# Kernel optimization log

Hardware: AMD Instinct MI355X
Metric: run time of the kernel (lower is better)

Reference implementation:

```python
import jax, jax.numpy as jnp
import numpy as np

D_MODEL = 512
HIDDEN = 2 * D_MODEL
B, L = 8, 2048
R_MIN, R_MAX = 0.8, 0.99
LN_EPS = 1e-5


def setup_inputs() -> dict:
    key = jax.random.key(0)
    ks = jax.random.split(key, 12)
    x = jax.random.normal(ks[0], (B, L, D_MODEL), jnp.float32)
    mask = jnp.ones((B, L), jnp.float32)
    # LRU eigenvalue init, exactly as the torch __init__
    u1 = jax.random.uniform(ks[1], (HIDDEN,), jnp.float32)
    u2 = jax.random.uniform(ks[2], (HIDDEN,), jnp.float32)
    nu_log = jnp.log(-0.5 * jnp.log(u1 * (R_MAX ** 2 - R_MIN ** 2) + R_MIN ** 2))
    theta_log = jnp.log(u2 * 2.0 * np.pi)
    diag_lambda = jnp.exp(jax.lax.complex(-jnp.exp(nu_log), jnp.exp(theta_log)))
    gamma_log = jnp.log(jnp.sqrt(1.0 - jnp.abs(diag_lambda) ** 2))
    params_log = jnp.stack([nu_log, theta_log, gamma_log])  # (3, HIDDEN)
    s_in = 1.0 / np.sqrt(D_MODEL)
    s_out = 1.0 / np.sqrt(HIDDEN)
    # complex Linear weights (real+imag parts; trained weights are fully complex)
    W_in_re = jax.random.uniform(ks[3], (HIDDEN, D_MODEL), jnp.float32, -s_in, s_in)
    W_in_im = jax.random.uniform(ks[4], (HIDDEN, D_MODEL), jnp.float32, -s_in, s_in)
    b_in_re = jax.random.uniform(ks[5], (HIDDEN,), jnp.float32, -s_in, s_in)
    b_in_im = jax.random.uniform(ks[6], (HIDDEN,), jnp.float32, -s_in, s_in)
    W_out_re = jax.random.uniform(ks[7], (D_MODEL, HIDDEN), jnp.float32, -s_out, s_out)
    W_out_im = jax.random.uniform(ks[8], (D_MODEL, HIDDEN), jnp.float32, -s_out, s_out)
    b_out_re = jax.random.uniform(ks[9], (D_MODEL,), jnp.float32, -s_out, s_out)
    b_out_im = jax.random.uniform(ks[10], (D_MODEL,), jnp.float32, -s_out, s_out)
    ln_w = jnp.ones((D_MODEL,), jnp.float32)
    ln_b = jnp.zeros((D_MODEL,), jnp.float32)
    return dict(x=x, mask=mask, params_log=params_log,
                W_in_re=W_in_re, W_in_im=W_in_im, b_in_re=b_in_re, b_in_im=b_in_im,
                W_out_re=W_out_re, W_out_im=W_out_im, b_out_re=b_out_re, b_out_im=b_out_im,
                ln_w=ln_w, ln_b=ln_b)


def _lru_parallel_scan(h, lamb, mask, Bn, Ln, Dn):
    # log-depth doubling trick over complex diagonal recurrence (faithful port)
    log2_L = int(np.ceil(np.log2(Ln)))
    for i in range(1, log2_L + 1):
        l = 2 ** i
        h = h.reshape(Bn * Ln // l, l, Dn)
        m = mask.reshape(Bn * Ln // l, l)
        h1, h2 = h[:, : l // 2], h[:, l // 2 :]
        if i > 1:
            lamb = jnp.concatenate([lamb, lamb * lamb[-1]], axis=0)  # powers lam^1..lam^(l/2)
        h2 = h2 + lamb * h1[:, -1:] * m[:, l // 2 - 1 : l // 2, None]
        h = jnp.concatenate([h1, h2], axis=1)
    return h.reshape(Bn, Ln, Dn)


def reference(x, mask, params_log, W_in_re, W_in_im, b_in_re, b_in_im,
              W_out_re, W_out_im, b_out_re, b_out_im, ln_w, ln_b):
    nu, theta, gamma = jnp.exp(params_log)  # each (HIDDEN,)
    lamb = jnp.exp(jax.lax.complex(-nu, theta))[None, :]  # (1, HIDDEN)
    W_in = jax.lax.complex(W_in_re, W_in_im)
    b_in = jax.lax.complex(b_in_re, b_in_im)
    W_out = jax.lax.complex(W_out_re, W_out_im)
    b_out = jax.lax.complex(b_out_re, b_out_im)
    xc = x.astype(jnp.complex64)
    h = (jnp.einsum('bld,hd->blh', xc, W_in) + b_in) * gamma  # (B, L, HIDDEN) complex64
    Bn, Ln, Dn = h.shape
    h = _lru_parallel_scan(h, lamb, mask, Bn, Ln, Dn)
    y = (jnp.einsum('blh,dh->bld', h, W_out) + b_out).real + x  # dropout = identity (eval)
    mean = jnp.mean(y, axis=-1, keepdims=True)
    var = jnp.var(y, axis=-1, keepdims=True)
    return (y - mean) / jnp.sqrt(var + LN_EPS) * ln_w + ln_b
```

## Files before the change

### kernel.cpp

```cpp
#include <hip/hip_runtime.h>
#include <hip/hip_bf16.h>
#include <cstdint>
#include <cstddef>


typedef unsigned short u16;
typedef __attribute__((ext_vector_type(8))) short bf16x8;
typedef __attribute__((ext_vector_type(4))) float f32x4;

#define B_    8
#define L_    2048
#define D_    512
#define H_    1024
#define M_    (B_ * L_)
#define SEG_  64
#define T_    (L_ / SEG_)

__device__ __forceinline__ float b2f(u16 u) {
  union { unsigned int i; float f; } v; v.i = ((unsigned int)u) << 16; return v.f;
}
__device__ __forceinline__ u16 f2b(float f) {
  union { float f; unsigned int i; } v; v.f = f;
  unsigned int x = v.i;
  return (u16)((x + 0x7fffu + ((x >> 16) & 1u)) >> 16);
}

__device__ __forceinline__ void gl2lds16(const void* g, void* l) {
  __builtin_amdgcn_global_load_lds(
      (const __attribute__((address_space(1))) void*)g,
      (__attribute__((address_space(3))) void*)l, 16, 0, 0);
}

__device__ __forceinline__ int ksw8(int row, int c) {
  return (c ^ (row & 7)) & 7;
}

__global__ __launch_bounds__(256) void conv_f32_bf16(
    const float* __restrict__ in, u16* __restrict__ out, int n4)
{
  int i = blockIdx.x * 256 + threadIdx.x;
  if (i < n4) {
    float4 v = ((const float4*)in)[i];
    ushort4 o;
    o.x = f2b(v.x); o.y = f2b(v.y); o.z = f2b(v.z); o.w = f2b(v.w);
    ((ushort4*)out)[i] = o;
  }
}

__global__ __launch_bounds__(256) void prep_weights(
    const float* __restrict__ wire, const float* __restrict__ wiim,
    const float* __restrict__ wore, const float* __restrict__ woim,
    const float* __restrict__ bire, const float* __restrict__ biim,
    const float* __restrict__ params,
    u16* __restrict__ winb, u16* __restrict__ wcat, float* __restrict__ bb)
{
  int i = blockIdx.x * 256 + threadIdx.x;
  float g = expf(params[2 * H_ + (i >> 9)]);
  winb[i]           = f2b(wire[i] * g);
  winb[H_ * D_ + i] = f2b(wiim[i] * g);
  int d = i >> 10, c = i & 1023;
  wcat[(size_t)d * 2048 + c]        = f2b(wore[i]);
  wcat[(size_t)d * 2048 + 1024 + c] = f2b(-woim[i]);
  if (i < 2048) {
    float gb = expf(params[2 * H_ + (i & (H_ - 1))]);
    bb[i] = ((i < 1024) ? bire[i] : biim[i - 1024]) * gb;
  }
}

template <int MODE>
__global__ __launch_bounds__(256, 3) void gemm_bt(
    const u16* __restrict__ A, const u16* __restrict__ Bp, int K,
    void* __restrict__ outp, int ldc, const float* __restrict__ p0)
{
  __shared__ __align__(16) u16 sA[128 * 64];
  __shared__ __align__(16) u16 sB[128 * 64];

  const int tid  = threadIdx.x;
  const int lane = tid & 63;
  const int wave = tid >> 6;
  const int wm = wave >> 1, wn = wave & 1;
  const int m0 = blockIdx.x * 128;
  const int n0 = blockIdx.y * 128;

  f32x4 acc[4][4];
#pragma unroll
  for (int i = 0; i < 4; ++i)
#pragma unroll
    for (int j = 0; j < 4; ++j) { f32x4 z = {0.f, 0.f, 0.f, 0.f}; acc[i][j] = z; }

  const int q = lane >> 4;
  const int r = lane & 15;

  for (int k0 = 0; k0 < K; k0 += 64) {
#pragma unroll
    for (int it = 0; it < 4; ++it) {
      int ci  = it * 256 + tid;
      int row = ci >> 3;
      int kc  = ksw8(row, ci & 7);
      gl2lds16(A  + (size_t)(m0 + row) * K + k0 + kc * 8, &sA[ci * 8]);
      gl2lds16(Bp + (size_t)(n0 + row) * K + k0 + kc * 8, &sB[ci * 8]);
    }
    __syncthreads();

#pragma unroll
    for (int kk = 0; kk < 2; ++kk) {
      const int cs = kk * 4 + q;
      bf16x8 af[4], bfv[4];
#pragma unroll
      for (int mt = 0; mt < 4; ++mt) {
        int arow = wm * 64 + mt * 16 + r;
        int slot = arow * 8 + ksw8(arow, cs);
        af[mt] = *(const bf16x8*)&sA[slot * 8];
      }
#pragma unroll
      for (int nt = 0; nt < 4; ++nt) {
        int brow = wn * 64 + nt * 16 + r;
        int slot = brow * 8 + ksw8(brow, cs);
        bfv[nt] = *(const bf16x8*)&sB[slot * 8];
      }
#pragma unroll
      for (int mt = 0; mt < 4; ++mt)
#pragma unroll
        for (int nt = 0; nt < 4; ++nt)
          acc[mt][nt] = __builtin_amdgcn_mfma_f32_16x16x32_bf16(
              bfv[nt], af[mt], acc[mt][nt], 0, 0, 0);
    }
    __syncthreads();
  }

#pragma unroll
  for (int nt = 0; nt < 4; ++nt) {
    const int nb4 = n0 + wn * 64 + nt * 16 + q * 4;
    const float4 b4 = *(const float4*)&p0[nb4];
#pragma unroll
    for (int mt = 0; mt < 4; ++mt) {
      const int mg = m0 + wm * 64 + mt * 16 + r;
      if (MODE == 0) {
        ushort4 o;
        o.x = f2b(acc[mt][nt][0] + b4.x);
        o.y = f2b(acc[mt][nt][1] + b4.y);
        o.z = f2b(acc[mt][nt][2] + b4.z);
        o.w = f2b(acc[mt][nt][3] + b4.w);
        *(ushort4*)&((u16*)outp)[(size_t)mg * ldc + nb4] = o;
      } else {
        float4 o;
        o.x = acc[mt][nt][0] + b4.x;
        o.y = acc[mt][nt][1] + b4.y;
        o.z = acc[mt][nt][2] + b4.z;
        o.w = acc[mt][nt][3] + b4.w;
        *(float4*)&((float*)outp)[(size_t)mg * ldc + nb4] = o;
      }
    }
  }
}

__global__ __launch_bounds__(256) void scan_fin(
    const u16* __restrict__ h, const float* __restrict__ mask,
    const float* __restrict__ params, float2* __restrict__ segfin,
    float* __restrict__ prodm)
{
  const int s = blockIdx.x, b = blockIdx.y;
  const int c4 = threadIdx.x * 4;
  float lr[4], li[4];
#pragma unroll
  for (int j = 0; j < 4; ++j) {
    int c = c4 + j;
    float nu = expf(params[c]);
    float th = expf(params[H_ + c]);
    float mg = expf(-nu);
    lr[j] = mg * cosf(th);
    li[j] = mg * sinf(th);
  }
  const int t0 = s * T_;
  const u16* p = h + (size_t)(b * L_ + t0) * (2 * H_) + c4;
  const float* mp = mask + b * L_ + t0;
  float fac0;
  if (t0 == 0) fac0 = 0.f; else fac0 = mask[b * L_ + t0 - 1];

  ushort4 bre[2][8], bim[2][8];
#pragma unroll
  for (int j = 0; j < 8; ++j) {
    bre[0][j] = *(const ushort4*)(p + (size_t)j * 2 * H_);
    bim[0][j] = *(const ushort4*)(p + (size_t)j * 2 * H_ + H_);
  }
  float sr[4] = {0, 0, 0, 0}, si[4] = {0, 0, 0, 0};
  float pm = 1.f;
#pragma unroll
  for (int ch = 0; ch < T_ / 8; ++ch) {
    const int cur = ch & 1, nxt = cur ^ 1;
    if (ch < T_ / 8 - 1) {
      const u16* pn = p + (size_t)(ch + 1) * 8 * 2 * H_;
#pragma unroll
      for (int j = 0; j < 8; ++j) {
        bre[nxt][j] = *(const ushort4*)(pn + (size_t)j * 2 * H_);
        bim[nxt][j] = *(const ushort4*)(pn + (size_t)j * 2 * H_ + H_);
      }
    }
#pragma unroll
    for (int j = 0; j < 8; ++j) {
      int i = ch * 8 + j;
      float fac = (i == 0) ? fac0 : mp[i - 1];
      pm *= fac;
      u16 rr[4], ii[4];
      *(ushort4*)rr = bre[cur][j]; *(ushort4*)ii = bim[cur][j];
#pragma unroll
      for (int k = 0; k < 4; ++k) {
        float ar = fac * sr[k], ai = fac * si[k];
        sr[k] = b2f(rr[k]) + lr[k] * ar - li[k] * ai;
        si[k] = b2f(ii[k]) + lr[k] * ai + li[k] * ar;
      }
    }
  }
#pragma unroll
  for (int j = 0; j < 4; ++j)
    segfin[(size_t)(b * SEG_ + s) * H_ + c4 + j] = make_float2(sr[j], si[j]);
  if (threadIdx.x == 0) prodm[b * SEG_ + s] = pm;
}

__global__ __launch_bounds__(256) void scan_carry(
    const float2* __restrict__ segfin, const float* __restrict__ prodm,
    const float* __restrict__ params, float2* __restrict__ carries)
{
  int idx = blockIdx.x * 256 + threadIdx.x;
  int b = idx >> 10, c = idx & 1023;
  float nu = expf(params[c]);
  float th = expf(params[H_ + c]);
  float mg = expf(-nu);
  float ltr = mg * cosf(th), lti = mg * sinf(th);
#pragma unroll
  for (int sq = 0; sq < 5; ++sq) {
    float nr = ltr * ltr - lti * lti;
    float ni = 2.f * ltr * lti;
    ltr = nr; lti = ni;
  }
  float cr = 0.f, ci = 0.f;
  float2 fin = segfin[(size_t)(b * SEG_) * H_ + c];
  float pmv = prodm[b * SEG_];
  for (int s = 0; s < SEG_; ++s) {
    size_t o = (size_t)(b * SEG_ + s) * H_ + c;
    carries[o] = make_float2(cr, ci);
    float2 finn; float pmn;
    if (s + 1 < SEG_) { finn = segfin[o + H_]; pmn = prodm[b * SEG_ + s + 1]; }
    float nr = fin.x + pmv * (ltr * cr - lti * ci);
    float ni = fin.y + pmv * (ltr * ci + lti * cr);
    cr = nr; ci = ni;
    fin = finn; pmv = pmn;
  }
}

__global__ __launch_bounds__(256) void scan_full(
    u16* __restrict__ h, const float* __restrict__ mask,
    const float* __restrict__ params, const float2* __restrict__ carries)
{
  const int s = blockIdx.x, b = blockIdx.y;
  const int c4 = threadIdx.x * 4;
  float lr[4], li[4], sr[4], si[4];
#pragma unroll
  for (int j = 0; j < 4; ++j) {
    int c = c4 + j;
    float nu = expf(params[c]);
    float th = expf(params[H_ + c]);
    float mg = expf(-nu);
    lr[j] = mg * cosf(th);
    li[j] = mg * sinf(th);
    float2 cv = carries[(size_t)(b * SEG_ + s) * H_ + c];
    sr[j] = cv.x; si[j] = cv.y;
  }
  const int t0 = s * T_;
  u16* p = h + (size_t)(b * L_ + t0) * (2 * H_) + c4;
  const float* mp = mask + b * L_ + t0;
  float fac0;
  if (t0 == 0) fac0 = 0.f; else fac0 = mask[b * L_ + t0 - 1];

  ushort4 bre[2][8], bim[2][8];
#pragma unroll
  for (int j = 0; j < 8; ++j) {
    bre[0][j] = *(const ushort4*)(p + (size_t)j * 2 * H_);
    bim[0][j] = *(const ushort4*)(p + (size_t)j * 2 * H_ + H_);
  }
#pragma unroll
  for (int ch = 0; ch < T_ / 8; ++ch) {
    const int cur = ch & 1, nxt = cur ^ 1;
    if (ch < T_ / 8 - 1) {
      const u16* pn = p + (size_t)(ch + 1) * 8 * 2 * H_;
#pragma unroll
      for (int j = 0; j < 8; ++j) {
        bre[nxt][j] = *(const ushort4*)(pn + (size_t)j * 2 * H_);
        bim[nxt][j] = *(const ushort4*)(pn + (size_t)j * 2 * H_ + H_);
      }
    }
#pragma unroll
    for (int j = 0; j < 8; ++j) {
      int i = ch * 8 + j;
      float fac = (i == 0) ? fac0 : mp[i - 1];
      u16 rr[4], ii[4], orr[4], oii[4];
      *(ushort4*)rr = bre[cur][j]; *(ushort4*)ii = bim[cur][j];
#pragma unroll
      for (int k = 0; k < 4; ++k) {
        float ar = fac * sr[k], ai = fac * si[k];
        float nr2 = b2f(rr[k]) + lr[k] * ar - li[k] * ai;
        float ni2 = b2f(ii[k]) + lr[k] * ai + li[k] * ar;
        sr[k] = nr2; si[k] = ni2;
        orr[k] = f2b(nr2); oii[k] = f2b(ni2);
      }
      *(ushort4*)(p + (size_t)i * 2 * H_)      = *(ushort4*)orr;
      *(ushort4*)(p + (size_t)i * 2 * H_ + H_) = *(ushort4*)oii;
    }
  }
}

__global__ __launch_bounds__(256) void ln_kernel(
    const float* __restrict__ y, const float* __restrict__ xg,
    const float* __restrict__ lnw, const float* __restrict__ lnb,
    float* __restrict__ out)
{
  const int wave = threadIdx.x >> 6, lane = threadIdx.x & 63;
  const size_t row = (size_t)blockIdx.x * 4 + wave;
  const float* yr = y + row * 512;
  const float* xr = xg + row * 512;
  float z[8];
  { float4 t = *(const float4*)&yr[lane * 4];        z[0]=t.x; z[1]=t.y; z[2]=t.z; z[3]=t.w; }
  { float4 t = *(const float4*)&yr[256 + lane * 4];  z[4]=t.x; z[5]=t.y; z[6]=t.z; z[7]=t.w; }
  { float4 t = *(const float4*)&xr[lane * 4];        z[0]+=t.x; z[1]+=t.y; z[2]+=t.z; z[3]+=t.w; }
  { float4 t = *(const float4*)&xr[256 + lane * 4];  z[4]+=t.x; z[5]+=t.y; z[6]+=t.z; z[7]+=t.w; }
  float s = 0.f, ss = 0.f;
#pragma unroll
  for (int j = 0; j < 8; ++j) { s += z[j]; ss += z[j] * z[j]; }
#pragma unroll
  for (int o = 32; o > 0; o >>= 1) { s += __shfl_xor(s, o); ss += __shfl_xor(ss, o); }
  const float mean = s * (1.f / 512.f);
  const float var  = ss * (1.f / 512.f) - mean * mean;
  const float inv  = rsqrtf(var + 1e-5f);
  float ov[8];
#pragma unroll
  for (int j = 0; j < 8; ++j) {
    int col = (j < 4) ? (lane * 4 + j) : (256 + lane * 4 + (j - 4));
    ov[j] = (z[j] - mean) * inv * lnw[col] + lnb[col];
  }
  { float4 t; t.x=ov[0]; t.y=ov[1]; t.z=ov[2]; t.w=ov[3];
    *(float4*)&out[row * 512 + lane * 4] = t; }
  { float4 t; t.x=ov[4]; t.y=ov[5]; t.z=ov[6]; t.w=ov[7];
    *(float4*)&out[row * 512 + 256 + lane * 4] = t; }
}

extern "C" void kernel_launch(void* const* d_in, const int* in_sizes, int n_in,
                              void* d_out, int out_size, void* d_ws, size_t ws_size,
                              hipStream_t stream) {
  (void)in_sizes; (void)n_in; (void)out_size; (void)ws_size;
  const float* x      = (const float*)d_in[0];
  const float* mask   = (const float*)d_in[1];
  const float* params = (const float*)d_in[2];
  const float* Wire   = (const float*)d_in[3];
  const float* Wiim   = (const float*)d_in[4];
  const float* bire   = (const float*)d_in[5];
  const float* biim   = (const float*)d_in[6];
  const float* Wore   = (const float*)d_in[7];
  const float* Woim   = (const float*)d_in[8];
  const float* bore   = (const float*)d_in[9];
  const float* lnw    = (const float*)d_in[11];
  const float* lnb    = (const float*)d_in[12];

  char* ws = (char*)d_ws;
  u16*    xb      = (u16*)   (ws);
  float2* segfin  = (float2*)(ws);
  float2* carries = (float2*)(ws + (size_t)4194304);
  float*  prodm   = (float*) (ws + (size_t)8388608);
  float*  y       = (float*) (ws);
  u16*    h       = (u16*)   (ws + (size_t)33554432);
  u16*    winb    = (u16*)   (ws + (size_t)100663296);
  u16*    wcat    = (u16*)   (ws + (size_t)102760448);
  float*  bb      = (float*) (ws + (size_t)104857600);

  conv_f32_bf16<<<8192, 256, 0, stream>>>(x, xb, M_ * D_ / 4);
  prep_weights<<<2048, 256, 0, stream>>>(Wire, Wiim, Wore, Woim, bire, biim,
                                         params, winb, wcat, bb);

  gemm_bt<0><<<dim3(128, 16), 256, 0, stream>>>(
      xb, winb, 512, (void*)h, 2048, bb);

  scan_fin<<<dim3(SEG_, B_), 256, 0, stream>>>(h, mask, params, segfin, prodm);
  scan_carry<<<32, 256, 0, stream>>>(segfin, prodm, params, carries);
  scan_full<<<dim3(SEG_, B_), 256, 0, stream>>>(h, mask, params, carries);

  gemm_bt<1><<<dim3(128, 4), 256, 0, stream>>>(
      h, wcat, 2048, (void*)y, 512, bore);

  ln_kernel<<<4096, 256, 0, stream>>>(y, x, lnw, lnb, (float*)d_out);
}
```

Before: 258.3 us.

## Fuse input conversion into weight prep and fold carry scan into scan_full

```diff
diff --git a/kernel.cpp b/kernel.cpp
--- a/kernel.cpp
+++ b/kernel.cpp
@@ -35,19 +35,8 @@
   return (c ^ (row & 7)) & 7;
 }
 
-__global__ __launch_bounds__(256) void conv_f32_bf16(
-    const float* __restrict__ in, u16* __restrict__ out, int n4)
-{
-  int i = blockIdx.x * 256 + threadIdx.x;
-  if (i < n4) {
-    float4 v = ((const float4*)in)[i];
-    ushort4 o;
-    o.x = f2b(v.x); o.y = f2b(v.y); o.z = f2b(v.z); o.w = f2b(v.w);
-    ((ushort4*)out)[i] = o;
-  }
-}
-
-__global__ __launch_bounds__(256) void prep_weights(
+__global__ __launch_bounds__(256) void prep_all(
+    const float* __restrict__ x, u16* __restrict__ xb,
     const float* __restrict__ wire, const float* __restrict__ wiim,
     const float* __restrict__ wore, const float* __restrict__ woim,
     const float* __restrict__ bire, const float* __restrict__ biim,
@@ -55,6 +44,14 @@
     u16* __restrict__ winb, u16* __restrict__ wcat, float* __restrict__ bb)
 {
   int i = blockIdx.x * 256 + threadIdx.x;
+#pragma unroll
+  for (int j = 0; j < 4; ++j) {
+    int gi = i + j * 524288;
+    float4 v = ((const float4*)x)[gi];
+    ushort4 o;
+    o.x = f2b(v.x); o.y = f2b(v.y); o.z = f2b(v.z); o.w = f2b(v.w);
+    ((ushort4*)xb)[gi] = o;
+  }
   float g = expf(params[2 * H_ + (i >> 9)]);
   winb[i]           = f2b(wire[i] * g);
   winb[H_ * D_ + i] = f2b(wiim[i] * g);
@@ -68,7 +65,7 @@
 }
 
 template <int MODE>
-__global__ __launch_bounds__(256, 3) void gemm_bt(
+__global__ __launch_bounds__(256, 4) void gemm_bt(
     const u16* __restrict__ A, const u16* __restrict__ Bp, int K,
     void* __restrict__ outp, int ldc, const float* __restrict__ p0)
 {
@@ -217,40 +214,10 @@
   if (threadIdx.x == 0) prodm[b * SEG_ + s] = pm;
 }
 
-__global__ __launch_bounds__(256) void scan_carry(
-    const float2* __restrict__ segfin, const float* __restrict__ prodm,
-    const float* __restrict__ params, float2* __restrict__ carries)
-{
-  int idx = blockIdx.x * 256 + threadIdx.x;
-  int b = idx >> 10, c = idx & 1023;
-  float nu = expf(params[c]);
-  float th = expf(params[H_ + c]);
-  float mg = expf(-nu);
-  float ltr = mg * cosf(th), lti = mg * sinf(th);
-#pragma unroll
-  for (int sq = 0; sq < 5; ++sq) {
-    float nr = ltr * ltr - lti * lti;
-    float ni = 2.f * ltr * lti;
-    ltr = nr; lti = ni;
-  }
-  float cr = 0.f, ci = 0.f;
-  float2 fin = segfin[(size_t)(b * SEG_) * H_ + c];
-  float pmv = prodm[b * SEG_];
-  for (int s = 0; s < SEG_; ++s) {
-    size_t o = (size_t)(b * SEG_ + s) * H_ + c;
-    carries[o] = make_float2(cr, ci);
-    float2 finn; float pmn;
-    if (s + 1 < SEG_) { finn = segfin[o + H_]; pmn = prodm[b * SEG_ + s + 1]; }
-    float nr = fin.x + pmv * (ltr * cr - lti * ci);
-    float ni = fin.y + pmv * (ltr * ci + lti * cr);
-    cr = nr; ci = ni;
-    fin = finn; pmv = pmn;
-  }
-}
-
 __global__ __launch_bounds__(256) void scan_full(
     u16* __restrict__ h, const float* __restrict__ mask,
-    const float* __restrict__ params, const float2* __restrict__ carries)
+    const float* __restrict__ params, const float2* __restrict__ segfin,
+    const float* __restrict__ prodm)
 {
   const int s = blockIdx.x, b = blockIdx.y;
   const int c4 = threadIdx.x * 4;
@@ -263,9 +230,31 @@
     float mg = expf(-nu);
     lr[j] = mg * cosf(th);
     li[j] = mg * sinf(th);
-    float2 cv = carries[(size_t)(b * SEG_ + s) * H_ + c];
-    sr[j] = cv.x; si[j] = cv.y;
-  }
+    sr[j] = 0.f; si[j] = 0.f;
+  }
+  float ltr[4], lti[4];
+#pragma unroll
+  for (int j = 0; j < 4; ++j) { ltr[j] = lr[j]; lti[j] = li[j]; }
+#pragma unroll
+  for (int sq = 0; sq < 5; ++sq)
+#pragma unroll
+    for (int j = 0; j < 4; ++j) {
+      float nr = ltr[j] * ltr[j] - lti[j] * lti[j];
+      float ni = 2.f * ltr[j] * lti[j];
+      ltr[j] = nr; lti[j] = ni;
+    }
+  for (int sp = 0; sp < s; ++sp) {
+    const float2* fp = &segfin[(size_t)(b * SEG_ + sp) * H_ + c4];
+    float pmv = prodm[b * SEG_ + sp];
+#pragma unroll
+    for (int j = 0; j < 4; ++j) {
+      float2 fin = fp[j];
+      float nr = fin.x + pmv * (ltr[j] * sr[j] - lti[j] * si[j]);
+      float ni = fin.y + pmv * (ltr[j] * si[j] + lti[j] * sr[j]);
+      sr[j] = nr; si[j] = ni;
+    }
+  }
+
   const int t0 = s * T_;
   u16* p = h + (size_t)(b * L_ + t0) * (2 * H_) + c4;
   const float* mp = mask + b * L_ + t0;
@@ -363,7 +352,6 @@
   char* ws = (char*)d_ws;
   u16*    xb      = (u16*)   (ws);
   float2* segfin  = (float2*)(ws);
-  float2* carries = (float2*)(ws + (size_t)4194304);
   float*  prodm   = (float*) (ws + (size_t)8388608);
   float*  y       = (float*) (ws);
   u16*    h       = (u16*)   (ws + (size_t)33554432);
@@ -371,16 +359,14 @@
   u16*    wcat    = (u16*)   (ws + (size_t)102760448);
   float*  bb      = (float*) (ws + (size_t)104857600);
 
-  conv_f32_bf16<<<8192, 256, 0, stream>>>(x, xb, M_ * D_ / 4);
-  prep_weights<<<2048, 256, 0, stream>>>(Wire, Wiim, Wore, Woim, bire, biim,
-                                         params, winb, wcat, bb);
+  prep_all<<<2048, 256, 0, stream>>>(x, xb, Wire, Wiim, Wore, Woim,
+                                     bire, biim, params, winb, wcat, bb);
 
   gemm_bt<0><<<dim3(128, 16), 256, 0, stream>>>(
       xb, winb, 512, (void*)h, 2048, bb);
 
   scan_fin<<<dim3(SEG_, B_), 256, 0, stream>>>(h, mask, params, segfin, prodm);
-  scan_carry<<<32, 256, 0, stream>>>(segfin, prodm, params, carries);
-  scan_full<<<dim3(SEG_, B_), 256, 0, stream>>>(h, mask, params, carries);
+  scan_full<<<dim3(SEG_, B_), 256, 0, stream>>>(h, mask, params, segfin, prodm);
 
   gemm_bt<1><<<dim3(128, 4), 256, 0, stream>>>(
       h, wcat, 2048, (void*)y, 512, bore);
```

Measured after the change: 261.7 us. Within noise of the previous version (+1.3%).
